# Optimization experiments

Hardware: AMD Instinct MI355X
Metric: run time of the kernel (lower is better)

The kernel has to match this reference:

```python
import jax, jax.numpy as jnp
import numpy as np

B, N, OBS, H, A = 1024, 64, 128, 256, 16
NH = 4
HD = H // NH


def _linear_params(key, fan_in, fan_out):
    k1, k2 = jax.random.split(key)
    bound = 1.0 / np.sqrt(fan_in)
    W = jax.random.uniform(k1, (fan_out, fan_in), jnp.float32, -bound, bound)
    b = jax.random.uniform(k2, (fan_out,), jnp.float32, -bound, bound)
    return W, b


def setup_inputs() -> dict:
    key = jax.random.key(0)
    ks = jax.random.split(key, 10)
    obs = jax.random.normal(ks[0], (B, N, OBS), jnp.float32)
    adj = jax.random.randint(ks[1], (B, N, N), 0, 2).astype(jnp.float32)
    # guarantee every row has at least one neighbor (self-loop) so softmax is finite
    adj = jnp.maximum(adj, jnp.eye(N, dtype=jnp.float32)[None])
    W1, b1 = _linear_params(ks[2], OBS, H)
    W2, b2 = _linear_params(ks[3], H, H)
    Wq, bq = _linear_params(ks[4], H, H)
    Wk, bk = _linear_params(ks[5], H, H)
    Wv, bv = _linear_params(ks[6], H, H)
    Wo, bo = _linear_params(ks[7], H, H)
    Wc, bc = _linear_params(ks[8], H, H)
    W3, b3 = _linear_params(ks[9], H, A)
    return dict(obs=obs, adj=adj, W1=W1, b1=b1, W2=W2, b2=b2,
                Wq=Wq, bq=bq, Wk=Wk, bk=bk, Wv=Wv, bv=bv,
                Wo=Wo, bo=bo, Wc=Wc, bc=bc, W3=W3, b3=b3)


def reference(obs, adj, W1, b1, W2, b2, Wq, bq, Wk, bk, Wv, bv, Wo, bo, Wc, bc, W3, b3):
    lin = lambda x, W, b: jnp.einsum('bnd,od->bno', x, W) + b
    x = jax.nn.relu(lin(obs, W1, b1))
    x = jax.nn.relu(lin(x, W2, b2))
    # multi-head attention with adjacency mask
    def heads(t):  # [B,N,H] -> [B,NH,N,HD]
        return t.reshape(B, N, NH, HD).transpose(0, 2, 1, 3)
    q = heads(lin(x, Wq, bq))
    k = heads(lin(x, Wk, bk))
    v = heads(lin(x, Wv, bv))
    scores = jnp.einsum('bhqd,bhkd->bhqk', q, k) / np.sqrt(HD).astype(np.float32)
    scores = jnp.where(adj[:, None] == 0, -jnp.inf, scores)
    attn = jax.nn.softmax(scores, axis=-1)
    out = jnp.einsum('bhqk,bhkd->bhqd', attn, v)
    out = out.transpose(0, 2, 1, 3).reshape(B, N, H)
    x = lin(out, Wo, bo)
    # communication: adj @ fc(x)
    x = jnp.einsum('bnm,bmh->bnh', adj, lin(x, Wc, bc))
    return lin(x, W3, b3)
```

## Files before the change

kernel.cpp:

```cpp
#include <hip/hip_runtime.h>
#include <stdint.h>

typedef unsigned short u16;
typedef unsigned long long u64;
typedef __attribute__((ext_vector_type(8))) short short8;
typedef __attribute__((ext_vector_type(4))) float f32x4;

#define MFMA16 __builtin_amdgcn_mfma_f32_16x16x32_bf16

#define B_ 1024
#define N_ 64
#define H_ 256
#define MTOT (B_ * N_)

__device__ __forceinline__ u16 f2bf(float f) {
  union { float f; uint32_t u; } v; v.f = f;
  uint32_t r = v.u + 0x7FFFu + ((v.u >> 16) & 1u);
  return (u16)(r >> 16);
}

union U8 { short8 v; u16 u[8]; };
union U4 { u64 v; u16 u[4]; };

__device__ __forceinline__ void cp16(const void* g, void* l) {
  __builtin_amdgcn_global_load_lds(
      (const __attribute__((address_space(1))) void*)g,
      (__attribute__((address_space(3))) void*)l, 16, 0, 0);
}

__global__ __launch_bounds__(256) void wconv(
    const float* __restrict__ W1, const float* __restrict__ W2,
    const float* __restrict__ Wq, const float* __restrict__ Wk,
    u16* o1, u16* o2, u16* oq, u16* ok) {
  int off8 = blockIdx.x * 256 + threadIdx.x;
  const float* src; u16* dst;
  if      (off8 <  4096) { src = W1; dst = o1; }
  else if (off8 < 12288) { src = W2; dst = o2; off8 -= 4096; }
  else if (off8 < 20480) { src = Wq; dst = oq; off8 -= 12288; }
  else                   { src = Wk; dst = ok; off8 -= 20480; }
  const int e = off8 * 8;
  f32x4 a = *(const f32x4*)(src + e);
  f32x4 b = *(const f32x4*)(src + e + 4);
  U8 pk;
#pragma unroll
  for (int j = 0; j < 4; j++) { pk.u[j] = f2bf(a[j]); pk.u[4 + j] = f2bf(b[j]); }
  *(short8*)(dst + e) = pk.v;
}

__global__ __launch_bounds__(256) void prep1(
    const float* __restrict__ Wc, const float* __restrict__ Wo,
    const float* __restrict__ bo, const float* __restrict__ bc,
    float* __restrict__ M1, float* __restrict__ bv) {
  const int j = blockIdx.x, d = threadIdx.x;
  __shared__ float wcr[256];
  __shared__ float red[4];
  wcr[d] = Wc[j * 256 + d];
  __syncthreads();
  float acc = 0.f;
  for (int i = 0; i < 256; i++) acc += wcr[i] * Wo[i * 256 + d];
  M1[j * 256 + d] = acc;
  float p = wcr[d] * bo[d];
  for (int off = 32; off >= 1; off >>= 1) p += __shfl_xor(p, off);
  if ((d & 63) == 0) red[d >> 6] = p;
  __syncthreads();
  if (d == 0) bv[j] = bc[j] + red[0] + red[1] + red[2] + red[3];
}

__global__ __launch_bounds__(256) void prep2(
    const float* __restrict__ W3, const float* __restrict__ M1,
    const float* __restrict__ bvchain, const float* __restrict__ bvw,
    float* __restrict__ Wzf, float* __restrict__ bz) {
  const int a = blockIdx.x, d = threadIdx.x;
  __shared__ float w3r[256];
  __shared__ float red[4];
  w3r[d] = W3[a * 256 + d];
  __syncthreads();
  float acc = 0.f;
  for (int j = 0; j < 256; j++) acc += w3r[j] * M1[j * 256 + d];
  Wzf[a * 256 + d] = acc;
  float p = w3r[d] * bvchain[d] + acc * bvw[d];
  for (int off = 32; off >= 1; off >>= 1) p += __shfl_xor(p, off);
  if ((d & 63) == 0) red[d >> 6] = p;
  __syncthreads();
  if (d == 0) bz[a] = red[0] + red[1] + red[2] + red[3];
}

__global__ __launch_bounds__(256) void prep3(
    const float* __restrict__ Wzf, const float* __restrict__ Wv,
    u16* __restrict__ G) {
  const int g = blockIdx.x, d2 = threadIdx.x;
  const int h = g >> 4, a = g & 15;
  __shared__ float wzr[64];
  if (d2 < 64) wzr[d2] = Wzf[a * 256 + h * 64 + d2];
  __syncthreads();
  float acc = 0.f;
#pragma unroll 8
  for (int d = 0; d < 64; d++) acc += wzr[d] * Wv[(size_t)(h * 64 + d) * 256 + d2];
  G[g * 256 + d2] = f2bf(acc);
}

__global__ __launch_bounds__(256, 2) void gemm1(
    const float* __restrict__ Af, const u16* __restrict__ Wb,
    const float* __restrict__ bias, u16* __restrict__ C) {
  __shared__ char smem[49152];
  u16* As = (u16*)smem;
  u16* Bs = (u16*)(smem + 16384);
  const int tid = threadIdx.x;
  const int lane = tid & 63, wid = tid >> 6;
  const int wr = wid >> 1, wc = wid & 1;
  const int ro = lane & 15, hi = lane >> 4;
  const int m0 = blockIdx.x * 128;
  const int K = 128;

  f32x4 acc[4][8];
#pragma unroll
  for (int m = 0; m < 4; m++)
#pragma unroll
    for (int n = 0; n < 8; n++) acc[m][n] = (f32x4){0.f, 0.f, 0.f, 0.f};

  for (int k0 = 0; k0 < K; k0 += 64) {
#pragma unroll
    for (int it = 0; it < 4; it++) {
      const int e = (tid + it * 256) * 8;
      const int r = e >> 6, c = e & 63;
      const float* s = Af + (size_t)(m0 + r) * K + k0 + c;
      f32x4 a = *(const f32x4*)s, b = *(const f32x4*)(s + 4);
      U8 pk;
#pragma unroll
      for (int j = 0; j < 4; j++) { pk.u[j] = f2bf(a[j]); pk.u[4 + j] = f2bf(b[j]); }
      *(short8*)&As[r * 64 + c] = pk.v;
    }
#pragma unroll
    for (int i = 0; i < 8; i++) {
      const int boff = i * 4096 + wid * 1024;
      const int loff = boff + lane * 16;
      const int r = loff >> 7, cb = loff & 127;
      cp16(Wb + (size_t)r * K + k0 + (cb >> 1), Bs + (boff >> 1));
    }
    __syncthreads();
#pragma unroll
    for (int kk = 0; kk < 64; kk += 32) {
      short8 af[4], bfr[8];
#pragma unroll
      for (int m = 0; m < 4; m++)
        af[m] = *(const short8*)&As[(wr * 64 + m * 16 + ro) * 64 + kk + hi * 8];
#pragma unroll
      for (int n = 0; n < 8; n++)
        bfr[n] = *(const short8*)&Bs[(wc * 128 + n * 16 + ro) * 64 + kk + hi * 8];
#pragma unroll
      for (int m = 0; m < 4; m++)
#pragma unroll
        for (int n = 0; n < 8; n++)
          acc[m][n] = MFMA16(af[m], bfr[n], acc[m][n], 0, 0, 0);
    }
    __syncthreads();
  }

  u16 (*Cs)[264] = (u16(*)[264])smem;
#pragma unroll
  for (int half = 0; half < 2; half++) {
    if (wr == half) {
#pragma unroll
      for (int n = 0; n < 8; n++) {
        const int col = wc * 128 + n * 16 + ro;
        const float bb = bias[col];
#pragma unroll
        for (int m = 0; m < 4; m++)
#pragma unroll
          for (int j = 0; j < 4; j++)
            Cs[m * 16 + hi * 4 + j][col] = f2bf(fmaxf(acc[m][n][j] + bb, 0.f));
      }
    }
    __syncthreads();
    for (int i = tid; i < 64 * 32; i += 256) {
      const int r = i >> 5, c = (i & 31) << 3;
      *(short8*)(C + (size_t)(m0 + half * 64 + r) * 256 + c) = *(short8*)&Cs[r][c];
    }
    __syncthreads();
  }
}

template<bool RELU>
__global__ __launch_bounds__(256, 2) void gemm_bt2(
    const u16* __restrict__ A,
    const u16* __restrict__ Wa, const float* __restrict__ ba, u16* __restrict__ Ca,
    const u16* __restrict__ Wb2, const float* __restrict__ bb2, u16* __restrict__ Cb2) {
  const u16* Wb = blockIdx.y ? Wb2 : Wa;
  const float* bias = blockIdx.y ? bb2 : ba;
  u16* C = blockIdx.y ? Cb2 : Ca;
  __shared__ char smem[49152];
  u16* As = (u16*)smem;
  u16* Bs = (u16*)(smem + 16384);
  const int tid = threadIdx.x;
  const int lane = tid & 63, wid = tid >> 6;
  const int wr = wid >> 1, wc = wid & 1;
  const int ro = lane & 15, hi = lane >> 4;
  const int m0 = blockIdx.x * 128;
  const int K = 256;

  f32x4 acc[4][8];
#pragma unroll
  for (int m = 0; m < 4; m++)
#pragma unroll
    for (int n = 0; n < 8; n++) acc[m][n] = (f32x4){0.f, 0.f, 0.f, 0.f};

  for (int k0 = 0; k0 < K; k0 += 64) {
#pragma unroll
    for (int i = 0; i < 4; i++) {
      const int boff = i * 4096 + wid * 1024;
      const int loff = boff + lane * 16;
      const int r = loff >> 7, cb = loff & 127;
      cp16(A + (size_t)(m0 + r) * K + k0 + (cb >> 1), As + (boff >> 1));
    }
#pragma unroll
    for (int i = 0; i < 8; i++) {
      const int boff = i * 4096 + wid * 1024;
      const int loff = boff + lane * 16;
      const int r = loff >> 7, cb = loff & 127;
      cp16(Wb + (size_t)r * K + k0 + (cb >> 1), Bs + (boff >> 1));
    }
    __syncthreads();
#pragma unroll
    for (int kk = 0; kk < 64; kk += 32) {
      short8 af[4], bfr[8];
#pragma unroll
      for (int m = 0; m < 4; m++)
        af[m] = *(const short8*)&As[(wr * 64 + m * 16 + ro) * 64 + kk + hi * 8];
#pragma unroll
      for (int n = 0; n < 8; n++)
        bfr[n] = *(const short8*)&Bs[(wc * 128 + n * 16 + ro) * 64 + kk + hi * 8];
#pragma unroll
      for (int m = 0; m < 4; m++)
#pragma unroll
        for (int n = 0; n < 8; n++)
          acc[m][n] = MFMA16(af[m], bfr[n], acc[m][n], 0, 0, 0);
    }
    __syncthreads();
  }

  u16 (*Cs)[264] = (u16(*)[264])smem;
#pragma unroll
  for (int half = 0; half < 2; half++) {
    if (wr == half) {
#pragma unroll
      for (int n = 0; n < 8; n++) {
        const int col = wc * 128 + n * 16 + ro;
        const float bb = bias[col];
#pragma unroll
        for (int m = 0; m < 4; m++)
#pragma unroll
          for (int j = 0; j < 4; j++) {
            float val = acc[m][n][j] + bb;
            if (RELU) val = fmaxf(val, 0.f);
            Cs[m * 16 + hi * 4 + j][col] = f2bf(val);
          }
      }
    }
    __syncthreads();
    for (int i = tid; i < 64 * 32; i += 256) {
      const int r = i >> 5, c = (i & 31) << 3;
      *(short8*)(C + (size_t)(m0 + half * 64 + r) * 256 + c) = *(short8*)&Cs[r][c];
    }
    __syncthreads();
  }
}

__global__ __launch_bounds__(256, 2) void gemmv(
    const u16* __restrict__ x2, const u16* __restrict__ G,
    u16* __restrict__ Vzt) {
  __shared__ char smem[49152];
  char* As = smem;
  char* Bs = smem + 16384;
  const int tid = threadIdx.x;
  const int lane = tid & 63, w = tid >> 6;
  const int ro = lane & 15, hi = lane >> 4;
  const int m0 = blockIdx.x * 128;

#pragma unroll
  for (int i = 0; i < 8; i++) {
    const int boff = i * 4096 + w * 1024;
    const int t = boff + lane * 16;
    const int row = t >> 9;
    const int cb = (t & 511) ^ ((row & 7) << 4);
    cp16(G + (size_t)row * 256 + (cb >> 1), Bs + boff);
  }

  f32x4 acc[2][4];
#pragma unroll
  for (int m = 0; m < 2; m++)
#pragma unroll
    for (int n = 0; n < 4; n++) acc[m][n] = (f32x4){0.f, 0.f, 0.f, 0.f};

  for (int k0 = 0; k0 < 256; k0 += 64) {
#pragma unroll
    for (int i = 0; i < 4; i++) {
      const int boff = i * 4096 + w * 1024;
      const int loff = boff + lane * 16;
      const int r = loff >> 7, cb = loff & 127;
      cp16(x2 + (size_t)(m0 + r) * 256 + k0 + (cb >> 1), As + boff);
    }
    __syncthreads();
#pragma unroll
    for (int kk = 0; kk < 64; kk += 32) {
      short8 af[2], bfr[4];
#pragma unroll
      for (int m = 0; m < 2; m++) {
        const int row = w * 32 + m * 16 + ro;
        af[m] = *(const short8*)(As + row * 128 + (kk + hi * 8) * 2);
      }
#pragma unroll
      for (int n = 0; n < 4; n++) {
        const int row = n * 16 + ro;
        bfr[n] = *(const short8*)(Bs + ((row * 512 + (k0 + kk + hi * 8) * 2) ^ ((row & 7) << 4)));
      }
#pragma unroll
      for (int m = 0; m < 2; m++)
#pragma unroll
        for (int n = 0; n < 4; n++)
          acc[m][n] = MFMA16(af[m], bfr[n], acc[m][n], 0, 0, 0);
    }
    __syncthreads();
  }

#pragma unroll
  for (int m = 0; m < 2; m++) {
    const int rbase = w * 32 + m * 16;
    const int bidx = (m0 >> 6) + (rbase >> 6);
    const int ke = (rbase + hi * 4) & 63;
#pragma unroll
    for (int n = 0; n < 4; n++) {
      const int c = n * 16 + ro;
      U4 pk;
#pragma unroll
      for (int j = 0; j < 4; j++) pk.u[j] = f2bf(acc[m][n][j]);
      *(u64*)(Vzt + (size_t)bidx * 4096 + (size_t)c * 64 + ke) = pk.v;
    }
  }
}

__global__ __launch_bounds__(256, 2) void attn_fused(
    const u16* __restrict__ Qg, const u16* __restrict__ Kg,
    const u16* __restrict__ Vzt, const float* __restrict__ adj,
    const float* __restrict__ bz, const float* __restrict__ b3,
    float* __restrict__ out) {
  __shared__ u16 Ps[4][64][72];
  __shared__ float Zs[4][64][16];
  __shared__ u64 adjm[64];
  __shared__ u16 chunk[64][4];

  const int b = blockIdx.x, tid = threadIdx.x;
  const int lane = tid & 63, w = tid >> 6;
  const int ro = lane & 15, hi = lane >> 4;
  const int hc = w * 64;
  const size_t base = (size_t)b * 64 * 256;

  short8 kb[4][2];
#pragma unroll
  for (int n = 0; n < 4; n++)
#pragma unroll
    for (int ks = 0; ks < 2; ks++)
      kb[n][ks] = *(const short8*)(Kg + base + (size_t)(n * 16 + ro) * 256 + hc + ks * 32 + hi * 8);

  {
    const int q = tid >> 2, qa = tid & 3;
    const float* ar = adj + ((size_t)b * 64 + q) * 64 + qa * 16;
    f32x4 a0 = *(const f32x4*)(ar);
    f32x4 a1 = *(const f32x4*)(ar + 4);
    f32x4 a2 = *(const f32x4*)(ar + 8);
    f32x4 a3 = *(const f32x4*)(ar + 12);
    unsigned m16 = 0;
#pragma unroll
    for (int i = 0; i < 4; i++) {
      m16 |= (unsigned)(a0[i] != 0.f) << i;
      m16 |= (unsigned)(a1[i] != 0.f) << (4 + i);
      m16 |= (unsigned)(a2[i] != 0.f) << (8 + i);
      m16 |= (unsigned)(a3[i] != 0.f) << (12 + i);
    }
    chunk[q][qa] = (u16)m16;
  }

  f32x4 s[4][4];
#pragma unroll
  for (int m = 0; m < 4; m++) {
    short8 af[2];
#pragma unroll
    for (int ks = 0; ks < 2; ks++)
      af[ks] = *(const short8*)(Qg + base + (size_t)(m * 16 + ro) * 256 + hc + ks * 32 + hi * 8);
#pragma unroll
    for (int n = 0; n < 4; n++) s[m][n] = (f32x4){0.f, 0.f, 0.f, 0.f};
#pragma unroll
    for (int ks = 0; ks < 2; ks++)
#pragma unroll
      for (int n = 0; n < 4; n++)
        s[m][n] = MFMA16(af[ks], kb[n][ks], s[m][n], 0, 0, 0);
  }

  short8 vz[2];
#pragma unroll
  for (int ks = 0; ks < 2; ks++)
    vz[ks] = *(const short8*)(Vzt + (size_t)b * 4096 + (size_t)(hc / 4 + ro) * 64 + ks * 32 + hi * 8);

  __syncthreads();
  if (tid < 64)
    adjm[tid] = (u64)chunk[tid][0] | ((u64)chunk[tid][1] << 16) |
                ((u64)chunk[tid][2] << 32) | ((u64)chunk[tid][3] << 48);
  __syncthreads();

#pragma unroll
  for (int m = 0; m < 4; m++) {
#pragma unroll
    for (int j = 0; j < 4; j++) {
      const int q = m * 16 + hi * 4 + j;
      const u64 msk = adjm[q];
      float sv[4], ev[4];
      float mx = -3.0e38f;
#pragma unroll
      for (int n = 0; n < 4; n++) {
        const bool on = (msk >> (n * 16 + ro)) & 1ull;
        sv[n] = on ? s[m][n][j] * 0.125f : -3.0e38f;
        mx = fmaxf(mx, sv[n]);
      }
      mx = fmaxf(mx, __shfl_xor(mx, 1));
      mx = fmaxf(mx, __shfl_xor(mx, 2));
      mx = fmaxf(mx, __shfl_xor(mx, 4));
      mx = fmaxf(mx, __shfl_xor(mx, 8));
      float sum = 0.f;
#pragma unroll
      for (int n = 0; n < 4; n++) {
        ev[n] = (sv[n] > -1.0e37f) ? __expf(sv[n] - mx) : 0.f;
        sum += ev[n];
      }
      sum += __shfl_xor(sum, 1);
      sum += __shfl_xor(sum, 2);
      sum += __shfl_xor(sum, 4);
      sum += __shfl_xor(sum, 8);
      const float inv = 1.0f / sum;
#pragma unroll
      for (int n = 0; n < 4; n++)
        Ps[w][q][n * 16 + ro] = f2bf(ev[n] * inv);
    }
  }

#pragma unroll
  for (int m = 0; m < 4; m++) {
    short8 pa[2];
    pa[0] = *(const short8*)&Ps[w][m * 16 + ro][hi * 8];
    pa[1] = *(const short8*)&Ps[w][m * 16 + ro][32 + hi * 8];
    f32x4 oz = (f32x4){0.f, 0.f, 0.f, 0.f};
#pragma unroll
    for (int ks = 0; ks < 2; ks++)
      oz = MFMA16(pa[ks], vz[ks], oz, 0, 0, 0);
#pragma unroll
    for (int j = 0; j < 4; j++)
      Zs[w][m * 16 + hi * 4 + j][ro] = oz[j];
  }
  __syncthreads();

  for (int i = tid; i < 1024; i += 256) {
    const int r = i >> 4, a = i & 15;
    Zs[0][r][a] += Zs[1][r][a] + Zs[2][r][a] + Zs[3][r][a];
  }
  __syncthreads();

  {
    const int n = tid >> 2, a4 = (tid & 3) << 2;
    const u64 msk = adjm[n];
    const float deg = (float)__popcll(msk);
    float a0 = 0.f, a1 = 0.f, a2 = 0.f, a3 = 0.f;
#pragma unroll 8
    for (int m = 0; m < 64; m++) {
      const float wv = (float)((msk >> m) & 1ull);
      f32x4 z = *(const f32x4*)&Zs[0][m][a4];
      a0 += wv * z[0]; a1 += wv * z[1]; a2 += wv * z[2]; a3 += wv * z[3];
    }
    f32x4 r;
    r[0] = a0 + b3[a4 + 0] + deg * bz[a4 + 0];
    r[1] = a1 + b3[a4 + 1] + deg * bz[a4 + 1];
    r[2] = a2 + b3[a4 + 2] + deg * bz[a4 + 2];
    r[3] = a3 + b3[a4 + 3] + deg * bz[a4 + 3];
    *(f32x4*)(out + ((size_t)b * 64 + n) * 16 + a4) = r;
  }
}

extern "C" void kernel_launch(void* const* d_in, const int* in_sizes, int n_in,
                              void* d_out, int out_size, void* d_ws, size_t ws_size,
                              hipStream_t stream) {
  const float* obs = (const float*)d_in[0];
  const float* adj = (const float*)d_in[1];
  const float* W1  = (const float*)d_in[2];
  const float* b1  = (const float*)d_in[3];
  const float* W2  = (const float*)d_in[4];
  const float* b2  = (const float*)d_in[5];
  const float* Wq  = (const float*)d_in[6];
  const float* bq  = (const float*)d_in[7];
  const float* Wk  = (const float*)d_in[8];
  const float* bk  = (const float*)d_in[9];
  const float* Wv  = (const float*)d_in[10];
  const float* bvw = (const float*)d_in[11];
  const float* Wo  = (const float*)d_in[12];
  const float* bo  = (const float*)d_in[13];
  const float* Wc  = (const float*)d_in[14];
  const float* bc  = (const float*)d_in[15];
  const float* W3  = (const float*)d_in[16];
  const float* b3  = (const float*)d_in[17];
  float* out = (float*)d_out;

  char* ws = (char*)d_ws;
  const size_t BIG = (size_t)MTOT * 256 * 2;
  u16* buf0 = (u16*)(ws);
  u16* buf1 = (u16*)(ws + BIG);
  u16* buf2 = (u16*)(ws + 2 * BIG);
  u16* buf3 = (u16*)(ws + 3 * BIG);
  char* p = ws + 4 * BIG;
  u16* W1b = (u16*)p;              p += 128 * 256 * 2;
  u16* W2b = (u16*)p;              p += 256 * 256 * 2;
  u16* Wqb = (u16*)p;              p += 256 * 256 * 2;
  u16* Wkb = (u16*)p;              p += 256 * 256 * 2;
  float* M1 = (float*)p;           p += 256 * 256 * 4;
  float* Wzf = (float*)p;          p += 16 * 256 * 4;
  u16* G   = (u16*)p;              p += 64 * 256 * 2;
  float* bv = (float*)p;           p += 256 * 4;
  float* bz = (float*)p;           p += 16 * 4;

  dim3 blk(256);
  wconv<<<dim3(112), blk, 0, stream>>>(W1, W2, Wq, Wk, W1b, W2b, Wqb, Wkb);
  prep1<<<dim3(256), blk, 0, stream>>>(Wc, Wo, bo, bc, M1, bv);
  prep2<<<dim3(16), blk, 0, stream>>>(W3, M1, bv, bvw, Wzf, bz);
  prep3<<<dim3(64), blk, 0, stream>>>(Wzf, Wv, G);

  gemm1<<<dim3(512), blk, 0, stream>>>(obs, W1b, b1, buf0);
  gemm_bt2<true ><<<dim3(512, 1), blk, 0, stream>>>(buf0, W2b, b2, buf1, W2b, b2, buf1);
  gemm_bt2<false><<<dim3(512, 2), blk, 0, stream>>>(buf1, Wqb, bq, buf2, Wkb, bk, buf3);
  gemmv<<<dim3(512), blk, 0, stream>>>(buf1, G, buf0);

  attn_fused<<<dim3(1024), blk, 0, stream>>>(buf2, buf3, buf0, adj, bz, b3, out);
}
```

Baseline: 140.5 us.

## Merge prep and GEMM launches into combined kernels with smaller swizzled tiles

Folds the small weight-prep kernels into the large GEMM launches as extra blocks, cutting the launch count from nine to five. The GEMMs move to 128x128 tiles with 32KB shared memory and higher occupancy (launch bounds 3-4 instead of 2), and gain XOR-swizzled LDS layouts to avoid bank conflicts. gemmv now streams G per k-step instead of preloading it. The risks are heterogeneous blocks running in one grid, and more A-tile reloads caused by the narrower N tiles.

```diff
diff --git a/kernel.cpp b/kernel.cpp
--- a/kernel.cpp
+++ b/kernel.cpp
@@ -10,7 +10,6 @@
 
 #define B_ 1024
 #define N_ 64
-#define H_ 256
 #define MTOT (B_ * N_)
 
 __device__ __forceinline__ u16 f2bf(float f) {
@@ -28,69 +27,247 @@
       (__attribute__((address_space(3))) void*)l, 16, 0, 0);
 }
 
-__global__ __launch_bounds__(256) void wconv(
+__global__ __launch_bounds__(256) void k_prep1_wconv(
+    const float* __restrict__ Wc, const float* __restrict__ Wo,
+    const float* __restrict__ bo, const float* __restrict__ bc,
+    float* __restrict__ M1, float* __restrict__ bv,
     const float* __restrict__ W1, const float* __restrict__ W2,
     const float* __restrict__ Wq, const float* __restrict__ Wk,
     u16* o1, u16* o2, u16* oq, u16* ok) {
-  int off8 = blockIdx.x * 256 + threadIdx.x;
-  const float* src; u16* dst;
-  if      (off8 <  4096) { src = W1; dst = o1; }
-  else if (off8 < 12288) { src = W2; dst = o2; off8 -= 4096; }
-  else if (off8 < 20480) { src = Wq; dst = oq; off8 -= 12288; }
-  else                   { src = Wk; dst = ok; off8 -= 20480; }
-  const int e = off8 * 8;
-  f32x4 a = *(const f32x4*)(src + e);
-  f32x4 b = *(const f32x4*)(src + e + 4);
-  U8 pk;
-#pragma unroll
-  for (int j = 0; j < 4; j++) { pk.u[j] = f2bf(a[j]); pk.u[4 + j] = f2bf(b[j]); }
-  *(short8*)(dst + e) = pk.v;
-}
-
-__global__ __launch_bounds__(256) void prep1(
-    const float* __restrict__ Wc, const float* __restrict__ Wo,
-    const float* __restrict__ bo, const float* __restrict__ bc,
-    float* __restrict__ M1, float* __restrict__ bv) {
-  const int j = blockIdx.x, d = threadIdx.x;
-  __shared__ float wcr[256];
-  __shared__ float red[4];
-  wcr[d] = Wc[j * 256 + d];
-  __syncthreads();
-  float acc = 0.f;
-  for (int i = 0; i < 256; i++) acc += wcr[i] * Wo[i * 256 + d];
-  M1[j * 256 + d] = acc;
-  float p = wcr[d] * bo[d];
-  for (int off = 32; off >= 1; off >>= 1) p += __shfl_xor(p, off);
-  if ((d & 63) == 0) red[d >> 6] = p;
-  __syncthreads();
-  if (d == 0) bv[j] = bc[j] + red[0] + red[1] + red[2] + red[3];
-}
-
-__global__ __launch_bounds__(256) void prep2(
+  const int bid = blockIdx.x, tid = threadIdx.x;
+  if (bid < 256) {
+    __shared__ float wcr[256];
+    __shared__ float red[4];
+    const int j = bid, d = tid;
+    wcr[d] = Wc[j * 256 + d];
+    __syncthreads();
+    float acc = 0.f;
+    for (int i = 0; i < 256; i++) acc += wcr[i] * Wo[i * 256 + d];
+    M1[j * 256 + d] = acc;
+    float p = wcr[d] * bo[d];
+    for (int off = 32; off >= 1; off >>= 1) p += __shfl_xor(p, off);
+    if ((d & 63) == 0) red[d >> 6] = p;
+    __syncthreads();
+    if (d == 0) bv[j] = bc[j] + red[0] + red[1] + red[2] + red[3];
+  } else {
+    int off8 = (bid - 256) * 256 + tid;
+    const float* src; u16* dst;
+    if      (off8 <  4096) { src = W1; dst = o1; }
+    else if (off8 < 12288) { src = W2; dst = o2; off8 -= 4096; }
+    else if (off8 < 20480) { src = Wq; dst = oq; off8 -= 12288; }
+    else                   { src = Wk; dst = ok; off8 -= 20480; }
+    const int e = off8 * 8;
+    f32x4 a = *(const f32x4*)(src + e);
+    f32x4 b = *(const f32x4*)(src + e + 4);
+    U8 pk;
+#pragma unroll
+    for (int j = 0; j < 4; j++) { pk.u[j] = f2bf(a[j]); pk.u[4 + j] = f2bf(b[j]); }
+    *(short8*)(dst + e) = pk.v;
+  }
+}
+
+__global__ __launch_bounds__(256, 3) void k_gemm1_prep2(
+    const float* __restrict__ obs, const u16* __restrict__ W1b,
+    const float* __restrict__ b1, u16* __restrict__ x1,
     const float* __restrict__ W3, const float* __restrict__ M1,
     const float* __restrict__ bvchain, const float* __restrict__ bvw,
     float* __restrict__ Wzf, float* __restrict__ bz) {
-  const int a = blockIdx.x, d = threadIdx.x;
-  __shared__ float w3r[256];
-  __shared__ float red[4];
-  w3r[d] = W3[a * 256 + d];
-  __syncthreads();
-  float acc = 0.f;
-  for (int j = 0; j < 256; j++) acc += w3r[j] * M1[j * 256 + d];
-  Wzf[a * 256 + d] = acc;
-  float p = w3r[d] * bvchain[d] + acc * bvw[d];
-  for (int off = 32; off >= 1; off >>= 1) p += __shfl_xor(p, off);
-  if ((d & 63) == 0) red[d >> 6] = p;
-  __syncthreads();
-  if (d == 0) bz[a] = red[0] + red[1] + red[2] + red[3];
-}
-
-__global__ __launch_bounds__(256) void prep3(
+  __shared__ char smem[49152];
+  const int tid = threadIdx.x;
+  if (blockIdx.x >= 512) {
+    float* w3r = (float*)smem;
+    float* red = (float*)(smem + 1024);
+    const int a = blockIdx.x - 512, d = tid;
+    w3r[d] = W3[a * 256 + d];
+    __syncthreads();
+    float acc = 0.f;
+    for (int j = 0; j < 256; j++) acc += w3r[j] * M1[j * 256 + d];
+    Wzf[a * 256 + d] = acc;
+    float p = w3r[d] * bvchain[d] + acc * bvw[d];
+    for (int off = 32; off >= 1; off >>= 1) p += __shfl_xor(p, off);
+    if ((d & 63) == 0) red[d >> 6] = p;
+    __syncthreads();
+    if (d == 0) bz[a] = red[0] + red[1] + red[2] + red[3];
+    return;
+  }
+  char* As = smem;
+  char* Bs = smem + 16384;
+  const int lane = tid & 63, wid = tid >> 6;
+  const int wr = wid >> 1, wc = wid & 1;
+  const int ro = lane & 15, hi = lane >> 4;
+  const int m0 = blockIdx.x * 128;
+
+  f32x4 acc[4][8];
+#pragma unroll
+  for (int m = 0; m < 4; m++)
+#pragma unroll
+    for (int n = 0; n < 8; n++) acc[m][n] = (f32x4){0.f, 0.f, 0.f, 0.f};
+
+  for (int k0 = 0; k0 < 128; k0 += 64) {
+#pragma unroll
+    for (int it = 0; it < 4; it++) {
+      const int e = (tid + it * 256) * 8;
+      const int r = e >> 6, c = e & 63;
+      const float* s = obs + (size_t)(m0 + r) * 128 + k0 + c;
+      f32x4 a = *(const f32x4*)s, b = *(const f32x4*)(s + 4);
+      U8 pk;
+#pragma unroll
+      for (int j = 0; j < 4; j++) { pk.u[j] = f2bf(a[j]); pk.u[4 + j] = f2bf(b[j]); }
+      *(short8*)(As + ((r * 128 + c * 2) ^ ((r & 7) << 4))) = pk.v;
+    }
+#pragma unroll
+    for (int i = 0; i < 8; i++) {
+      const int boff = i * 4096 + wid * 1024;
+      const int t = boff + lane * 16;
+      const int row = t >> 7;
+      const int cb = (t & 127) ^ ((row & 7) << 4);
+      cp16(W1b + (size_t)row * 128 + k0 + (cb >> 1), Bs + boff);
+    }
+    __syncthreads();
+#pragma unroll
+    for (int kk = 0; kk < 64; kk += 32) {
+      short8 af[4], bfr[8];
+#pragma unroll
+      for (int m = 0; m < 4; m++) {
+        const int row = wr * 64 + m * 16 + ro;
+        af[m] = *(const short8*)(As + ((row * 128 + (kk + hi * 8) * 2) ^ ((row & 7) << 4)));
+      }
+#pragma unroll
+      for (int n = 0; n < 8; n++) {
+        const int row = wc * 128 + n * 16 + ro;
+        bfr[n] = *(const short8*)(Bs + ((row * 128 + (kk + hi * 8) * 2) ^ ((row & 7) << 4)));
+      }
+#pragma unroll
+      for (int m = 0; m < 4; m++)
+#pragma unroll
+        for (int n = 0; n < 8; n++)
+          acc[m][n] = MFMA16(af[m], bfr[n], acc[m][n], 0, 0, 0);
+    }
+    __syncthreads();
+  }
+
+  u16 (*Cs)[264] = (u16(*)[264])smem;
+#pragma unroll
+  for (int half = 0; half < 2; half++) {
+    if (wr == half) {
+#pragma unroll
+      for (int n = 0; n < 8; n++) {
+        const int col = wc * 128 + n * 16 + ro;
+        const float bb = b1[col];
+#pragma unroll
+        for (int m = 0; m < 4; m++)
+#pragma unroll
+          for (int j = 0; j < 4; j++)
+            Cs[m * 16 + hi * 4 + j][col] = f2bf(fmaxf(acc[m][n][j] + bb, 0.f));
+      }
+    }
+    __syncthreads();
+    for (int i = tid; i < 64 * 32; i += 256) {
+      const int r = i >> 5, c = (i & 31) << 3;
+      *(short8*)(x1 + (size_t)(m0 + half * 64 + r) * 256 + c) = *(short8*)&Cs[r][c];
+    }
+    __syncthreads();
+  }
+}
+
+__device__ __forceinline__ void gemm128(
+    const u16* __restrict__ A, const u16* __restrict__ W,
+    const float* __restrict__ bias, u16* __restrict__ C,
+    const int m0, const int n0, const bool relu, char* smem) {
+  char* As = smem;
+  char* Bs = smem + 16384;
+  const int tid = threadIdx.x;
+  const int lane = tid & 63, wid = tid >> 6;
+  const int wr = wid >> 1, wc = wid & 1;
+  const int ro = lane & 15, hi = lane >> 4;
+
+  f32x4 acc[4][4];
+#pragma unroll
+  for (int m = 0; m < 4; m++)
+#pragma unroll
+    for (int n = 0; n < 4; n++) acc[m][n] = (f32x4){0.f, 0.f, 0.f, 0.f};
+
+  for (int k0 = 0; k0 < 256; k0 += 64) {
+#pragma unroll
+    for (int i = 0; i < 4; i++) {
+      const int boff = i * 4096 + wid * 1024;
+      const int t = boff + lane * 16;
+      const int row = t >> 7;
+      const int cb = (t & 127) ^ ((row & 7) << 4);
+      cp16(A + (size_t)(m0 + row) * 256 + k0 + (cb >> 1), As + boff);
+    }
+#pragma unroll
+    for (int i = 0; i < 4; i++) {
+      const int boff = i * 4096 + wid * 1024;
+      const int t = boff + lane * 16;
+      const int row = t >> 7;
+      const int cb = (t & 127) ^ ((row & 7) << 4);
+      cp16(W + (size_t)(n0 + row) * 256 + k0 + (cb >> 1), Bs + boff);
+    }
+    __syncthreads();
+#pragma unroll
+    for (int kk = 0; kk < 64; kk += 32) {
+      short8 af[4], bfr[4];
+#pragma unroll
+      for (int m = 0; m < 4; m++) {
+        const int row = wr * 64 + m * 16 + ro;
+        af[m] = *(const short8*)(As + ((row * 128 + (kk + hi * 8) * 2) ^ ((row & 7) << 4)));
+      }
+#pragma unroll
+      for (int n = 0; n < 4; n++) {
+        const int row = wc * 64 + n * 16 + ro;
+        bfr[n] = *(const short8*)(Bs + ((row * 128 + (kk + hi * 8) * 2) ^ ((row & 7) << 4)));
+      }
+#pragma unroll
+      for (int m = 0; m < 4; m++)
+#pragma unroll
+        for (int n = 0; n < 4; n++)
+          acc[m][n] = MFMA16(af[m], bfr[n], acc[m][n], 0, 0, 0);
+    }
+    __syncthreads();
+  }
+
+  u16 (*Cs)[136] = (u16(*)[136])smem;
+#pragma unroll
+  for (int half = 0; half < 2; half++) {
+    if (wr == half) {
+#pragma unroll
+      for (int n = 0; n < 4; n++) {
+        const int col = wc * 64 + n * 16 + ro;
+        const float bb = bias[n0 + col];
+#pragma unroll
+        for (int m = 0; m < 4; m++)
+#pragma unroll
+          for (int j = 0; j < 4; j++) {
+            float val = acc[m][n][j] + bb;
+            if (relu) val = fmaxf(val, 0.f);
+            Cs[m * 16 + hi * 4 + j][col] = f2bf(val);
+          }
+      }
+    }
+    __syncthreads();
+    for (int i = tid; i < 64 * 16; i += 256) {
+      const int r = i >> 4, c = (i & 15) << 3;
+      *(short8*)(C + (size_t)(m0 + half * 64 + r) * 256 + n0 + c) = *(short8*)&Cs[r][c];
+    }
+    __syncthreads();
+  }
+}
+
+__global__ __launch_bounds__(256, 4) void k_x2_prep3(
+    const u16* __restrict__ x1, const u16* __restrict__ W2b,
+    const float* __restrict__ b2, u16* __restrict__ x2,
     const float* __restrict__ Wzf, const float* __restrict__ Wv,
     u16* __restrict__ G) {
-  const int g = blockIdx.x, d2 = threadIdx.x;
+  __shared__ char smem[32768];
+  if (blockIdx.x < 1024) {
+    gemm128(x1, W2b, b2, x2, (blockIdx.x >> 1) * 128, (blockIdx.x & 1) * 128,
+            true, smem);
+    return;
+  }
+  const int g = blockIdx.x - 1024, d2 = threadIdx.x;
   const int h = g >> 4, a = g & 15;
-  __shared__ float wzr[64];
+  float* wzr = (float*)smem;
   if (d2 < 64) wzr[d2] = Wzf[a * 256 + h * 64 + d2];
   __syncthreads();
   float acc = 0.f;
@@ -99,191 +276,25 @@
   G[g * 256 + d2] = f2bf(acc);
 }
 
-__global__ __launch_bounds__(256, 2) void gemm1(
-    const float* __restrict__ Af, const u16* __restrict__ Wb,
-    const float* __restrict__ bias, u16* __restrict__ C) {
-  __shared__ char smem[49152];
-  u16* As = (u16*)smem;
-  u16* Bs = (u16*)(smem + 16384);
-  const int tid = threadIdx.x;
-  const int lane = tid & 63, wid = tid >> 6;
-  const int wr = wid >> 1, wc = wid & 1;
-  const int ro = lane & 15, hi = lane >> 4;
-  const int m0 = blockIdx.x * 128;
-  const int K = 128;
-
-  f32x4 acc[4][8];
-#pragma unroll
-  for (int m = 0; m < 4; m++)
-#pragma unroll
-    for (int n = 0; n < 8; n++) acc[m][n] = (f32x4){0.f, 0.f, 0.f, 0.f};
-
-  for (int k0 = 0; k0 < K; k0 += 64) {
-#pragma unroll
-    for (int it = 0; it < 4; it++) {
-      const int e = (tid + it * 256) * 8;
-      const int r = e >> 6, c = e & 63;
-      const float* s = Af + (size_t)(m0 + r) * K + k0 + c;
-      f32x4 a = *(const f32x4*)s, b = *(const f32x4*)(s + 4);
-      U8 pk;
-#pragma unroll
-      for (int j = 0; j < 4; j++) { pk.u[j] = f2bf(a[j]); pk.u[4 + j] = f2bf(b[j]); }
-      *(short8*)&As[r * 64 + c] = pk.v;
-    }
-#pragma unroll
-    for (int i = 0; i < 8; i++) {
-      const int boff = i * 4096 + wid * 1024;
-      const int loff = boff + lane * 16;
-      const int r = loff >> 7, cb = loff & 127;
-      cp16(Wb + (size_t)r * K + k0 + (cb >> 1), Bs + (boff >> 1));
-    }
-    __syncthreads();
-#pragma unroll
-    for (int kk = 0; kk < 64; kk += 32) {
-      short8 af[4], bfr[8];
-#pragma unroll
-      for (int m = 0; m < 4; m++)
-        af[m] = *(const short8*)&As[(wr * 64 + m * 16 + ro) * 64 + kk + hi * 8];
-#pragma unroll
-      for (int n = 0; n < 8; n++)
-        bfr[n] = *(const short8*)&Bs[(wc * 128 + n * 16 + ro) * 64 + kk + hi * 8];
-#pragma unroll
-      for (int m = 0; m < 4; m++)
-#pragma unroll
-        for (int n = 0; n < 8; n++)
-          acc[m][n] = MFMA16(af[m], bfr[n], acc[m][n], 0, 0, 0);
-    }
-    __syncthreads();
-  }
-
-  u16 (*Cs)[264] = (u16(*)[264])smem;
-#pragma unroll
-  for (int half = 0; half < 2; half++) {
-    if (wr == half) {
-#pragma unroll
-      for (int n = 0; n < 8; n++) {
-        const int col = wc * 128 + n * 16 + ro;
-        const float bb = bias[col];
-#pragma unroll
-        for (int m = 0; m < 4; m++)
-#pragma unroll
-          for (int j = 0; j < 4; j++)
-            Cs[m * 16 + hi * 4 + j][col] = f2bf(fmaxf(acc[m][n][j] + bb, 0.f));
-      }
-    }
-    __syncthreads();
-    for (int i = tid; i < 64 * 32; i += 256) {
-      const int r = i >> 5, c = (i & 31) << 3;
-      *(short8*)(C + (size_t)(m0 + half * 64 + r) * 256 + c) = *(short8*)&Cs[r][c];
-    }
-    __syncthreads();
-  }
-}
-
-template<bool RELU>
-__global__ __launch_bounds__(256, 2) void gemm_bt2(
-    const u16* __restrict__ A,
-    const u16* __restrict__ Wa, const float* __restrict__ ba, u16* __restrict__ Ca,
-    const u16* __restrict__ Wb2, const float* __restrict__ bb2, u16* __restrict__ Cb2) {
-  const u16* Wb = blockIdx.y ? Wb2 : Wa;
-  const float* bias = blockIdx.y ? bb2 : ba;
-  u16* C = blockIdx.y ? Cb2 : Ca;
-  __shared__ char smem[49152];
-  u16* As = (u16*)smem;
-  u16* Bs = (u16*)(smem + 16384);
-  const int tid = threadIdx.x;
-  const int lane = tid & 63, wid = tid >> 6;
-  const int wr = wid >> 1, wc = wid & 1;
-  const int ro = lane & 15, hi = lane >> 4;
-  const int m0 = blockIdx.x * 128;
-  const int K = 256;
-
-  f32x4 acc[4][8];
-#pragma unroll
-  for (int m = 0; m < 4; m++)
-#pragma unroll
-    for (int n = 0; n < 8; n++) acc[m][n] = (f32x4){0.f, 0.f, 0.f, 0.f};
-
-  for (int k0 = 0; k0 < K; k0 += 64) {
-#pragma unroll
-    for (int i = 0; i < 4; i++) {
-      const int boff = i * 4096 + wid * 1024;
-      const int loff = boff + lane * 16;
-      const int r = loff >> 7, cb = loff & 127;
-      cp16(A + (size_t)(m0 + r) * K + k0 + (cb >> 1), As + (boff >> 1));
-    }
-#pragma unroll
-    for (int i = 0; i < 8; i++) {
-      const int boff = i * 4096 + wid * 1024;
-      const int loff = boff + lane * 16;
-      const int r = loff >> 7, cb = loff & 127;
-      cp16(Wb + (size_t)r * K + k0 + (cb >> 1), Bs + (boff >> 1));
-    }
-    __syncthreads();
-#pragma unroll
-    for (int kk = 0; kk < 64; kk += 32) {
-      short8 af[4], bfr[8];
-#pragma unroll
-      for (int m = 0; m < 4; m++)
-        af[m] = *(const short8*)&As[(wr * 64 + m * 16 + ro) * 64 + kk + hi * 8];
-#pragma unroll
-      for (int n = 0; n < 8; n++)
-        bfr[n] = *(const short8*)&Bs[(wc * 128 + n * 16 + ro) * 64 + kk + hi * 8];
-#pragma unroll
-      for (int m = 0; m < 4; m++)
-#pragma unroll
-        for (int n = 0; n < 8; n++)
-          acc[m][n] = MFMA16(af[m], bfr[n], acc[m][n], 0, 0, 0);
-    }
-    __syncthreads();
-  }
-
-  u16 (*Cs)[264] = (u16(*)[264])smem;
-#pragma unroll
-  for (int half = 0; half < 2; half++) {
-    if (wr == half) {
-#pragma unroll
-      for (int n = 0; n < 8; n++) {
-        const int col = wc * 128 + n * 16 + ro;
-        const float bb = bias[col];
-#pragma unroll
-        for (int m = 0; m < 4; m++)
-#pragma unroll
-          for (int j = 0; j < 4; j++) {
-            float val = acc[m][n][j] + bb;
-            if (RELU) val = fmaxf(val, 0.f);
-            Cs[m * 16 + hi * 4 + j][col] = f2bf(val);
-          }
-      }
-    }
-    __syncthreads();
-    for (int i = tid; i < 64 * 32; i += 256) {
-      const int r = i >> 5, c = (i & 31) << 3;
-      *(short8*)(C + (size_t)(m0 + half * 64 + r) * 256 + c) = *(short8*)&Cs[r][c];
-    }
-    __syncthreads();
-  }
-}
-
-__global__ __launch_bounds__(256, 2) void gemmv(
-    const u16* __restrict__ x2, const u16* __restrict__ G,
-    u16* __restrict__ Vzt) {
-  __shared__ char smem[49152];
+__global__ __launch_bounds__(256, 4) void k_qk_gemmv(
+    const u16* __restrict__ x2,
+    const u16* __restrict__ Wqb, const float* __restrict__ bq, u16* __restrict__ Qg,
+    const u16* __restrict__ Wkb, const float* __restrict__ bk, u16* __restrict__ Kg,
+    const u16* __restrict__ G, u16* __restrict__ Vzt) {
+  __shared__ char smem[32768];
+  const int bid = blockIdx.x;
+  if (bid < 2048) {
+    const int which = bid & 1;
+    gemm128(x2, which ? Wkb : Wqb, which ? bk : bq, which ? Kg : Qg,
+            (bid >> 2) * 128, ((bid >> 1) & 1) * 128, false, smem);
+    return;
+  }
   char* As = smem;
   char* Bs = smem + 16384;
   const int tid = threadIdx.x;
   const int lane = tid & 63, w = tid >> 6;
   const int ro = lane & 15, hi = lane >> 4;
-  const int m0 = blockIdx.x * 128;
-
-#pragma unroll
-  for (int i = 0; i < 8; i++) {
-    const int boff = i * 4096 + w * 1024;
-    const int t = boff + lane * 16;
-    const int row = t >> 9;
-    const int cb = (t & 511) ^ ((row & 7) << 4);
-    cp16(G + (size_t)row * 256 + (cb >> 1), Bs + boff);
-  }
+  const int m0 = (bid - 2048) * 128;
 
   f32x4 acc[2][4];
 #pragma unroll
@@ -295,9 +306,22 @@
 #pragma unroll
     for (int i = 0; i < 4; i++) {
       const int boff = i * 4096 + w * 1024;
-      const int loff = boff + lane * 16;
-      const int r = loff >> 7, cb = loff & 127;
-      cp16(x2 + (size_t)(m0 + r) * 256 + k0 + (cb >> 1), As + boff);
+      const int t = boff + lane * 16;
+      const int row = t >> 7;
+      const int cb = (t & 127) ^ ((row & 7) << 4);
+      cp16(x2 + (size_t)(m0 + row) * 256 + k0 + (cb >> 1), As + boff);
+    }
+    {
+      const int boff = w * 1024;
+      const int t = boff + lane * 16;
+      const int row = t >> 7;
+      const int cb = (t & 127) ^ ((row & 7) << 4);
+      cp16(G + (size_t)row * 256 + k0 + (cb >> 1), Bs + boff);
+      const int boff2 = 4096 + w * 1024;
+      const int t2 = boff2 + lane * 16;
+      const int row2 = t2 >> 7;
+      const int cb2 = (t2 & 127) ^ ((row2 & 7) << 4);
+      cp16(G + (size_t)row2 * 256 + k0 + (cb2 >> 1), Bs + boff2);
     }
     __syncthreads();
 #pragma unroll
@@ -306,12 +330,12 @@
 #pragma unroll
       for (int m = 0; m < 2; m++) {
         const int row = w * 32 + m * 16 + ro;
-        af[m] = *(const short8*)(As + row * 128 + (kk + hi * 8) * 2);
+        af[m] = *(const short8*)(As + ((row * 128 + (kk + hi * 8) * 2) ^ ((row & 7) << 4)));
       }
 #pragma unroll
       for (int n = 0; n < 4; n++) {
         const int row = n * 16 + ro;
-        bfr[n] = *(const short8*)(Bs + ((row * 512 + (k0 + kk + hi * 8) * 2) ^ ((row & 7) << 4)));
+        bfr[n] = *(const short8*)(Bs + ((row * 128 + (kk + hi * 8) * 2) ^ ((row & 7) << 4)));
       }
 #pragma unroll
       for (int m = 0; m < 2; m++)
@@ -523,15 +547,12 @@
   float* bz = (float*)p;           p += 16 * 4;
 
   dim3 blk(256);
-  wconv<<<dim3(112), blk, 0, stream>>>(W1, W2, Wq, Wk, W1b, W2b, Wqb, Wkb);
-  prep1<<<dim3(256), blk, 0, stream>>>(Wc, Wo, bo, bc, M1, bv);
-  prep2<<<dim3(16), blk, 0, stream>>>(W3, M1, bv, bvw, Wzf, bz);
-  prep3<<<dim3(64), blk, 0, stream>>>(Wzf, Wv, G);
-
-  gemm1<<<dim3(512), blk, 0, stream>>>(obs, W1b, b1, buf0);
-  gemm_bt2<true ><<<dim3(512, 1), blk, 0, stream>>>(buf0, W2b, b2, buf1, W2b, b2, buf1);
-  gemm_bt2<false><<<dim3(512, 2), blk, 0, stream>>>(buf1, Wqb, bq, buf2, Wkb, bk, buf3);
-  gemmv<<<dim3(512), blk, 0, stream>>>(buf1, G, buf0);
-
+  k_prep1_wconv<<<dim3(368), blk, 0, stream>>>(Wc, Wo, bo, bc, M1, bv,
+                                               W1, W2, Wq, Wk, W1b, W2b, Wqb, Wkb);
+  k_gemm1_prep2<<<dim3(528), blk, 0, stream>>>(obs, W1b, b1, buf0,
+                                               W3, M1, bv, bvw, Wzf, bz);
+  k_x2_prep3<<<dim3(1088), blk, 0, stream>>>(buf0, W2b, b2, buf1, Wzf, Wv, G);
+  k_qk_gemmv<<<dim3(2560), blk, 0, stream>>>(buf1, Wqb, bq, buf2,
+                                             Wkb, bk, buf3, G, buf0);
   attn_fused<<<dim3(1024), blk, 0, stream>>>(buf2, buf3, buf0, adj, bz, b3, out);
 }
```

Result: slower. 154.8 us (+10.2%).
